# Optimization experiments

Measured on AMD Instinct MI355X. Metric: run time of the kernel, lower is better.

Reference implementation:

```python
import jax, jax.numpy as jnp
import numpy as np

N, F, H, E, R = 100000, 256, 64, 800000, 7
EPS = 1e-5

def _layernorm(x, g, b):
    mu = jnp.mean(x, axis=-1, keepdims=True)
    var = jnp.mean((x - mu) ** 2, axis=-1, keepdims=True)
    return (x - mu) * jax.lax.rsqrt(var + EPS) * g + b

def setup_inputs() -> dict:
    key = jax.random.key(0)
    ks = jax.random.split(key, 16)
    block_features = jax.random.normal(ks[0], (N, F), dtype=jnp.float32)
    src = jax.random.randint(ks[1], (E,), 0, N).astype(jnp.float32)
    dst = jax.random.randint(ks[2], (E,), 0, N).astype(jnp.float32)
    rel = jax.random.randint(ks[3], (E,), 0, R).astype(jnp.float32)
    w = jax.random.uniform(ks[4], (E,), dtype=jnp.float32)
    typed_edges = jnp.stack([src, dst, rel, w], axis=1)  # [E,4]
    def lin(k, fan_in, fan_out):
        s = 1.0 / np.sqrt(fan_in)
        k1, k2 = jax.random.split(k)
        return (jax.random.uniform(k1, (fan_in, fan_out), jnp.float32, -s, s),
                jax.random.uniform(k2, (fan_out,), jnp.float32, -s, s))
    W1, b1 = lin(ks[5], F, H)
    W2, b2 = lin(ks[6], H, H)
    rel_emb = jax.random.normal(ks[7], (R, H), dtype=jnp.float32)
    Wm1, bm1 = lin(ks[8], 3 * H + 1, H)
    Wm2, bm2 = lin(ks[9], H, H)
    Wg1, bg1 = lin(ks[10], 2 * H, H)
    Wg2, bg2 = lin(ks[11], H, H)
    return dict(block_features=block_features, typed_edges=typed_edges,
                W1=W1, b1=b1, g1=jnp.ones(H), be1=jnp.zeros(H), W2=W2, b2=b2,
                rel_emb=rel_emb, Wm1=Wm1, bm1=bm1, Wm2=Wm2, bm2=bm2,
                gn=jnp.ones(H), bn=jnp.zeros(H), Wg1=Wg1, bg1=bg1, Wg2=Wg2, bg2=bg2)

def reference(block_features, typed_edges, W1, b1, g1, be1, W2, b2, rel_emb,
              Wm1, bm1, Wm2, bm2, gn, bn, Wg1, bg1, Wg2, bg2):
    # node_proj: Linear -> LN -> ReLU -> Linear -> ReLU
    h = jax.nn.relu(_layernorm(block_features @ W1 + b1, g1, be1))
    h = jax.nn.relu(h @ W2 + b2)  # [N,H]
    src = typed_edges[:, 0].astype(jnp.int32)
    dst = typed_edges[:, 1].astype(jnp.int32)
    rel = typed_edges[:, 2].astype(jnp.int32)
    w = typed_edges[:, 3:4]  # [E,1]
    m_in = jnp.concatenate([h[src], h[dst], rel_emb[rel], w], axis=-1)  # [E,3H+1]
    msg = jax.nn.relu(m_in @ Wm1 + bm1) @ Wm2 + bm2  # [E,H]
    agg = jax.ops.segment_sum(msg, dst, num_segments=h.shape[0])  # [N,H]
    nodes = _layernorm(h + agg, gn, bn)
    g = jnp.concatenate([nodes.mean(axis=0), nodes.max(axis=0)], axis=-1)  # [2H]
    return jax.nn.relu(g @ Wg1 + bg1) @ Wg2 + bg2  # [H]
```

## Files before the change

kernel.cpp:

```cpp
#include <hip/hip_runtime.h>

typedef unsigned short u16;
typedef unsigned int   u32;
typedef __attribute__((ext_vector_type(8))) short bf16x8;
typedef __attribute__((ext_vector_type(4))) float f32x4;

#define EPS 1e-5f
#define MFMA(a,b,c) __builtin_amdgcn_mfma_f32_16x16x32_bf16(a,b,c,0,0,0)

constexpr int OB_b1=0, OB_g1=64, OB_be1=128, OB_b2=192, OB_bm1=256, OB_w192=320,
              OB_bm2=384, OB_gn=448, OB_bn=512, OB_bg1=576, OB_bg2=640,
              OB_Wg1=704, OB_Wg2=8896, WB_TOT=12992;
constexpr int FR_Wm1=0;
constexpr int FR_Wm2=12288;
constexpr int FR_rel=16384;
constexpr int FR_W1 =16960;
constexpr int FR_W2 =33344;
constexpr int FR_TOT=37440;

__device__ __forceinline__ float bf2f(u32 u) { return __uint_as_float(u << 16); }
__device__ __forceinline__ u16 f2bf(float f) {
  u32 b = __float_as_uint(f);
  return (u16)((b + 0x7fffu + ((b >> 16) & 1u)) >> 16);
}
__device__ __forceinline__ u32 fkey(float f) {
  u32 b = __float_as_uint(f);
  return (b & 0x80000000u) ? ~b : (b | 0x80000000u);
}

__launch_bounds__(256)
__global__ void k_prep(const float* __restrict__ W1, const float* __restrict__ b1,
                       const float* __restrict__ g1, const float* __restrict__ be1,
                       const float* __restrict__ W2, const float* __restrict__ b2,
                       const float* __restrict__ rel_emb,
                       const float* __restrict__ Wm1, const float* __restrict__ bm1,
                       const float* __restrict__ Wm2, const float* __restrict__ bm2,
                       const float* __restrict__ gn, const float* __restrict__ bn,
                       const float* __restrict__ Wg1, const float* __restrict__ bg1,
                       const float* __restrict__ Wg2, const float* __restrict__ bg2,
                       float* __restrict__ wbuf, u16* __restrict__ frags) {
  int tid = blockIdx.x * 256 + threadIdx.x;
  int nth = gridDim.x * 256;
  for (int i = tid; i < 64; i += nth) {
    wbuf[OB_b1 + i] = b1[i];   wbuf[OB_g1 + i] = g1[i];
    wbuf[OB_be1 + i] = be1[i]; wbuf[OB_b2 + i] = b2[i];
    wbuf[OB_bm1 + i] = bm1[i]; wbuf[OB_w192 + i] = Wm1[192 * 64 + i];
    wbuf[OB_bm2 + i] = bm2[i]; wbuf[OB_gn + i] = gn[i];
    wbuf[OB_bn + i] = bn[i];   wbuf[OB_bg1 + i] = bg1[i];
    wbuf[OB_bg2 + i] = bg2[i];
  }
  for (int i = tid; i < 8192; i += nth) wbuf[OB_Wg1 + i] = Wg1[i];
  for (int i = tid; i < 4096; i += nth) wbuf[OB_Wg2 + i] = Wg2[i];
  for (int idx = tid; idx < 16384; idx += nth) {
    int f = idx >> 9, L = (idx >> 3) & 63, j = idx & 7;
    int k = (f >> 2) * 32 + ((L >> 4) << 3) + j, n = ((f & 3) << 4) + (L & 15);
    frags[FR_W1 + idx] = f2bf(W1[k * 64 + n]);
  }
  for (int idx = tid; idx < 4096; idx += nth) {
    int f = idx >> 9, L = (idx >> 3) & 63, j = idx & 7;
    int k = (f >> 2) * 32 + ((L >> 4) << 3) + j, n = ((f & 3) << 4) + (L & 15);
    frags[FR_W2 + idx] = f2bf(W2[k * 64 + n]);
  }
  for (int idx = tid; idx < 12288; idx += nth) {
    int f = idx >> 9, L = (idx >> 3) & 63, j = idx & 7;
    int k = (f >> 2) * 32 + ((L >> 4) << 3) + j, n = ((f & 3) << 4) + (L & 15);
    frags[FR_Wm1 + idx] = f2bf(Wm1[k * 64 + n]);
  }
  for (int idx = tid; idx < 4096; idx += nth) {
    int f = idx >> 9, L = (idx >> 3) & 63, j = idx & 7;
    int k = (f >> 2) * 32 + ((L >> 4) << 3) + j, n = ((f & 3) << 4) + (L & 15);
    frags[FR_Wm2 + idx] = f2bf(Wm2[k * 64 + n]);
  }
  for (int idx = tid; idx < 576; idx += nth) {
    int r = idx / 80, c = idx % 80;
    frags[FR_rel + idx] = (r < 7 && c < 64) ? f2bf(rel_emb[r * 64 + c]) : (u16)0;
  }
}

__launch_bounds__(256, 3)
__global__ void k_h(const float* __restrict__ X, const float* __restrict__ wbuf,
                    const u16* __restrict__ frags, u16* __restrict__ hb, int N) {
  __shared__ __align__(16) u16 sW1[32 * 512];
  __shared__ __align__(16) u16 sW2[8 * 512];
  __shared__ __align__(16) u16 st[4][16 * 72];

  {
    const uint4* srcp = (const uint4*)(frags + FR_W1);
    uint4* d1 = (uint4*)sW1;
    for (int i = threadIdx.x; i < 2048; i += 256) d1[i] = srcp[i];
    const uint4* srcp2 = (const uint4*)(frags + FR_W2);
    uint4* d2 = (uint4*)sW2;
    for (int i = threadIdx.x; i < 512; i += 256) d2[i] = srcp2[i];
  }
  __syncthreads();

  int lane = threadIdx.x & 63, wave = threadIdx.x >> 6;
  int m = lane & 15, quad = lane >> 4, koff = quad * 8, col0 = m;

  float b1v[4], g1v[4], be1v[4], b2v[4];
  #pragma unroll
  for (int nt = 0; nt < 4; nt++) {
    int c = nt * 16 + col0;
    b1v[nt] = wbuf[OB_b1 + c]; g1v[nt] = wbuf[OB_g1 + c];
    be1v[nt] = wbuf[OB_be1 + c]; b2v[nt] = wbuf[OB_b2 + c];
  }

  int ntiles = (N + 15) / 16;
  int wid = blockIdx.x * 4 + wave, nw = gridDim.x * 4;
  for (int tile = wid; tile < ntiles; tile += nw) {
    int n0 = tile * 16;
    int nm = min(n0 + m, N - 1);
    const float* xr = X + (size_t)nm * 256 + koff;

    f32x4 acc[4] = {};
    #pragma unroll 1
    for (int ks = 0; ks < 8; ks++) {
      float4 u0 = *(const float4*)(xr + ks * 32);
      float4 u1 = *(const float4*)(xr + ks * 32 + 4);
      bf16x8 a;
      a[0] = (short)f2bf(u0.x); a[1] = (short)f2bf(u0.y);
      a[2] = (short)f2bf(u0.z); a[3] = (short)f2bf(u0.w);
      a[4] = (short)f2bf(u1.x); a[5] = (short)f2bf(u1.y);
      a[6] = (short)f2bf(u1.z); a[7] = (short)f2bf(u1.w);
      #pragma unroll
      for (int nt = 0; nt < 4; nt++) {
        bf16x8 b = *(const bf16x8*)(sW1 + (ks * 4 + nt) * 512 + lane * 8);
        acc[nt] = MFMA(a, b, acc[nt]);
      }
    }

    float v[4][4];
    #pragma unroll
    for (int nt = 0; nt < 4; nt++)
      #pragma unroll
      for (int r = 0; r < 4; r++) v[nt][r] = acc[nt][r] + b1v[nt];

    #pragma unroll
    for (int r = 0; r < 4; r++) {
      float s = v[0][r] + v[1][r] + v[2][r] + v[3][r];
      #pragma unroll
      for (int mk = 8; mk >= 1; mk >>= 1) s += __shfl_xor(s, mk, 64);
      float mu = s * (1.f / 64.f);
      float q = 0.f;
      #pragma unroll
      for (int nt = 0; nt < 4; nt++) { float d = v[nt][r] - mu; q += d * d; }
      #pragma unroll
      for (int mk = 8; mk >= 1; mk >>= 1) q += __shfl_xor(q, mk, 64);
      float rs = rsqrtf(q * (1.f / 64.f) + EPS);
      #pragma unroll
      for (int nt = 0; nt < 4; nt++) {
        float h1 = fmaxf(fmaf((v[nt][r] - mu) * rs, g1v[nt], be1v[nt]), 0.f);
        st[wave][(quad * 4 + r) * 72 + nt * 16 + col0] = f2bf(h1);
      }
    }
    __builtin_amdgcn_wave_barrier();

    f32x4 acc2[4] = {};
    #pragma unroll
    for (int ks = 0; ks < 2; ks++) {
      bf16x8 a2 = *(const bf16x8*)(st[wave] + m * 72 + ks * 32 + koff);
      #pragma unroll
      for (int nt = 0; nt < 4; nt++) {
        bf16x8 b = *(const bf16x8*)(sW2 + (ks * 4 + nt) * 512 + lane * 8);
        acc2[nt] = MFMA(a2, b, acc2[nt]);
      }
    }
    __builtin_amdgcn_wave_barrier();

    #pragma unroll
    for (int nt = 0; nt < 4; nt++)
      #pragma unroll
      for (int r = 0; r < 4; r++) {
        int row = n0 + quad * 4 + r;
        if (row < N)
          hb[(size_t)row * 64 + nt * 16 + col0] = f2bf(fmaxf(acc2[nt][r] + b2v[nt], 0.f));
      }
  }
}

__launch_bounds__(256, 3)
__global__ void k_edge(const float* __restrict__ te, const u16* __restrict__ hb,
                       const float* __restrict__ wbuf, const u16* __restrict__ frags,
                       float* __restrict__ agg, int E, int N) {
  __shared__ __align__(16) u16 sWm1[24 * 512];
  __shared__ __align__(16) u16 sWm2[8 * 512];
  __shared__ __align__(16) u16 srel[576];
  __shared__ __align__(16) u16 st[4][16 * 72];

  {
    const uint4* s1 = (const uint4*)(frags + FR_Wm1);
    uint4* d1 = (uint4*)sWm1;
    for (int i = threadIdx.x; i < 1536; i += 256) d1[i] = s1[i];
    const uint4* s2 = (const uint4*)(frags + FR_Wm2);
    uint4* d2 = (uint4*)sWm2;
    for (int i = threadIdx.x; i < 512; i += 256) d2[i] = s2[i];
    const uint4* s3 = (const uint4*)(frags + FR_rel);
    uint4* d3 = (uint4*)srel;
    for (int i = threadIdx.x; i < 72; i += 256) d3[i] = s3[i];
  }
  __syncthreads();

  int lane = threadIdx.x & 63, wave = threadIdx.x >> 6;
  int m = lane & 15, quad = lane >> 4, koff = quad * 8, col0 = m;

  float bm1v[4], w192v[4], bm2v[4];
  #pragma unroll
  for (int nt = 0; nt < 4; nt++) {
    int c = nt * 16 + col0;
    bm1v[nt] = wbuf[OB_bm1 + c];
    w192v[nt] = wbuf[OB_w192 + c];
    bm2v[nt] = wbuf[OB_bm2 + c];
  }

  int ntiles = (E + 15) / 16;
  int wid = blockIdx.x * 4 + wave, nw = gridDim.x * 4;
  for (int tile = wid; tile < ntiles; tile += nw) {
    int e0 = tile * 16;
    int src = 0, dst = 0, rel = 0; float w = 0.f;
    if (lane < 16) {
      int e = min(e0 + lane, E - 1);
      float4 v = *(const float4*)(te + (size_t)e * 4);
      src = min(max((int)v.x, 0), N - 1);
      dst = min(max((int)v.y, 0), N - 1);
      rel = min(max((int)v.z, 0), 6);
      w = v.w;
    }
    int src_m = __shfl(src, m, 64);
    int dst_m = __shfl(dst, m, 64);
    int rel_m = __shfl(rel, m, 64);

    const u16* hs = hb + (size_t)src_m * 64;
    const u16* hd = hb + (size_t)dst_m * 64;
    bf16x8 af[6];
    af[0] = *(const bf16x8*)(hs + koff);
    af[1] = *(const bf16x8*)(hs + 32 + koff);
    af[2] = *(const bf16x8*)(hd + koff);
    af[3] = *(const bf16x8*)(hd + 32 + koff);
    af[4] = *(const bf16x8*)(srel + rel_m * 80 + koff);
    af[5] = *(const bf16x8*)(srel + rel_m * 80 + 32 + koff);

    f32x4 acc[4] = {};
    #pragma unroll
    for (int ks = 0; ks < 6; ks++) {
      #pragma unroll
      for (int nt = 0; nt < 4; nt++) {
        bf16x8 b = *(const bf16x8*)(sWm1 + (ks * 4 + nt) * 512 + lane * 8);
        acc[nt] = MFMA(af[ks], b, acc[nt]);
      }
    }

    float wrow[4];
    #pragma unroll
    for (int r = 0; r < 4; r++) wrow[r] = __shfl(w, quad * 4 + r, 64);
    #pragma unroll
    for (int nt = 0; nt < 4; nt++)
      #pragma unroll
      for (int r = 0; r < 4; r++) {
        float v = fmaf(wrow[r], w192v[nt], acc[nt][r] + bm1v[nt]);
        st[wave][(quad * 4 + r) * 72 + nt * 16 + col0] = f2bf(fmaxf(v, 0.f));
      }
    __builtin_amdgcn_wave_barrier();

    f32x4 acc2[4] = {};
    #pragma unroll
    for (int ks = 0; ks < 2; ks++) {
      bf16x8 a2 = *(const bf16x8*)(st[wave] + m * 72 + ks * 32 + koff);
      #pragma unroll
      for (int nt = 0; nt < 4; nt++) {
        bf16x8 b = *(const bf16x8*)(sWm2 + (ks * 4 + nt) * 512 + lane * 8);
        acc2[nt] = MFMA(a2, b, acc2[nt]);
      }
    }
    __builtin_amdgcn_wave_barrier();

    int dstr[4]; bool valr[4];
    #pragma unroll
    for (int r = 0; r < 4; r++) {
      int row = quad * 4 + r;
      dstr[r] = __shfl(dst, row, 64);
      valr[r] = (e0 + row) < E;
    }
    #pragma unroll
    for (int nt = 0; nt < 4; nt++)
      #pragma unroll
      for (int r = 0; r < 4; r++)
        if (valr[r])
          atomicAdd(agg + (size_t)dstr[r] * 64 + nt * 16 + col0, acc2[nt][r] + bm2v[nt]);
  }
}

__launch_bounds__(256)
__global__ void k_nodes(const u16* __restrict__ hb, const float* __restrict__ agg,
                        const float* __restrict__ wbuf, float* __restrict__ gsum,
                        u32* __restrict__ gmax, int N) {
  int lane = threadIdx.x & 63, wave = threadIdx.x >> 6;
  int wid = blockIdx.x * 4 + wave;
  int nw = gridDim.x * 4;
  float gn = wbuf[OB_gn + lane], bn = wbuf[OB_bn + lane];
  float sj = 0.f, mj = -3.0e38f;
  for (int n = wid; n < N; n += nw) {
    float v = bf2f(hb[(size_t)n * 64 + lane]) + agg[(size_t)n * 64 + lane];
    float s = v;
    #pragma unroll
    for (int m = 32; m >= 1; m >>= 1) s += __shfl_xor(s, m, 64);
    float mu = s * (1.f / 64.f);
    float d = v - mu;
    float q = d * d;
    #pragma unroll
    for (int m = 32; m >= 1; m >>= 1) q += __shfl_xor(q, m, 64);
    float rs = rsqrtf(q * (1.f / 64.f) + EPS);
    float val = fmaf(d * rs, gn, bn);
    sj += val;
    mj = fmaxf(mj, val);
  }
  __shared__ float bs[256], bm[256];
  bs[threadIdx.x] = sj;
  bm[threadIdx.x] = mj;
  __syncthreads();
  if (threadIdx.x < 64) {
    int t = threadIdx.x;
    float ts = bs[t] + bs[64 + t] + bs[128 + t] + bs[192 + t];
    float tm = fmaxf(fmaxf(bm[t], bm[64 + t]), fmaxf(bm[128 + t], bm[192 + t]));
    atomicAdd(gsum + t, ts);
    atomicMax(gmax + t, fkey(tm));
  }
}

__launch_bounds__(128)
__global__ void k_final(const float* __restrict__ wbuf, const float* __restrict__ gsum,
                        const u32* __restrict__ gmax, float* __restrict__ out, int N) {
  __shared__ float g[128];
  __shared__ float y1[64];
  int t = threadIdx.x;
  if (t < 64) {
    g[t] = gsum[t] / (float)N;
  } else {
    u32 k = gmax[t - 64];
    u32 b = (k & 0x80000000u) ? (k & 0x7fffffffu) : ~k;
    g[t] = __uint_as_float(b);
  }
  __syncthreads();
  if (t < 64) {
    float a = wbuf[OB_bg1 + t];
    for (int i = 0; i < 128; i++) a = fmaf(g[i], wbuf[OB_Wg1 + i * 64 + t], a);
    y1[t] = fmaxf(a, 0.f);
  }
  __syncthreads();
  if (t < 64) {
    float a = wbuf[OB_bg2 + t];
    for (int k = 0; k < 64; k++) a = fmaf(y1[k], wbuf[OB_Wg2 + k * 64 + t], a);
    out[t] = a;
  }
}

extern "C" void kernel_launch(void* const* d_in, const int* in_sizes, int n_in,
                              void* d_out, int out_size, void* d_ws, size_t ws_size,
                              hipStream_t stream) {
  const int N = in_sizes[0] / 256;
  const int E = in_sizes[1] / 4;

  char* ws = (char*)d_ws;
  size_t aggB = (size_t)N * 64 * 4;
  size_t hbB  = (size_t)N * 64 * 2;
  float* agg   = (float*)ws;
  u16*   hb    = (u16*)(ws + aggB);
  float* gsum  = (float*)(ws + aggB + hbB);
  u32*   gmax  = (u32*)(ws + aggB + hbB + 256);
  float* wbuf  = (float*)(ws + aggB + hbB + 512);
  u16*   frags = (u16*)(ws + aggB + hbB + 512 + (size_t)WB_TOT * 4);

  const float* X  = (const float*)d_in[0];
  const float* te = (const float*)d_in[1];

  hipLaunchKernelGGL(k_prep, dim3(64), dim3(256), 0, stream,
                     (const float*)d_in[2], (const float*)d_in[3], (const float*)d_in[4],
                     (const float*)d_in[5], (const float*)d_in[6], (const float*)d_in[7],
                     (const float*)d_in[8], (const float*)d_in[9], (const float*)d_in[10],
                     (const float*)d_in[11], (const float*)d_in[12], (const float*)d_in[13],
                     (const float*)d_in[14], (const float*)d_in[15], (const float*)d_in[16],
                     (const float*)d_in[17], (const float*)d_in[18], wbuf, frags);
  hipMemsetAsync(agg, 0, aggB, stream);
  hipMemsetAsync(gsum, 0, 512, stream);
  hipLaunchKernelGGL(k_h, dim3(640), dim3(256), 0, stream, X, wbuf, frags, hb, N);
  hipLaunchKernelGGL(k_edge, dim3(768), dim3(256), 0, stream, te, hb, wbuf, frags, agg, E, N);
  hipLaunchKernelGGL(k_nodes, dim3(2048), dim3(256), 0, stream, hb, agg, wbuf, gsum, gmax, N);
  hipLaunchKernelGGL(k_final, dim3(1), dim3(128), 0, stream, wbuf, gsum, gmax, (float*)d_out, N);
}
```

Baseline: 442.6 us.

## Sort edges by destination and reduce runs before scattering aggregates

Edges are counted per destination, prefix-scanned and permuted into destination order. Each wave then accumulates contiguous same-destination messages in registers and issues one store or atomic per run, replacing one atomic per element. The prep kernel is dropped: weights are swizzled into shared memory inside each consumer kernel, the final MLP is folded into the last block of the node kernel, and the memsets are merged into one. The risk is the extra count, scan and permute passes, a single-block serial scan over 100k nodes, and messages rounded to bf16 before summation.

```diff
diff --git a/kernel.cpp b/kernel.cpp
--- a/kernel.cpp
+++ b/kernel.cpp
@@ -8,16 +8,6 @@
 #define EPS 1e-5f
 #define MFMA(a,b,c) __builtin_amdgcn_mfma_f32_16x16x32_bf16(a,b,c,0,0,0)
 
-constexpr int OB_b1=0, OB_g1=64, OB_be1=128, OB_b2=192, OB_bm1=256, OB_w192=320,
-              OB_bm2=384, OB_gn=448, OB_bn=512, OB_bg1=576, OB_bg2=640,
-              OB_Wg1=704, OB_Wg2=8896, WB_TOT=12992;
-constexpr int FR_Wm1=0;
-constexpr int FR_Wm2=12288;
-constexpr int FR_rel=16384;
-constexpr int FR_W1 =16960;
-constexpr int FR_W2 =33344;
-constexpr int FR_TOT=37440;
-
 __device__ __forceinline__ float bf2f(u32 u) { return __uint_as_float(u << 16); }
 __device__ __forceinline__ u16 f2bf(float f) {
   u32 b = __float_as_uint(f);
@@ -28,70 +18,28 @@
   return (b & 0x80000000u) ? ~b : (b | 0x80000000u);
 }
 
-__launch_bounds__(256)
-__global__ void k_prep(const float* __restrict__ W1, const float* __restrict__ b1,
-                       const float* __restrict__ g1, const float* __restrict__ be1,
-                       const float* __restrict__ W2, const float* __restrict__ b2,
-                       const float* __restrict__ rel_emb,
-                       const float* __restrict__ Wm1, const float* __restrict__ bm1,
-                       const float* __restrict__ Wm2, const float* __restrict__ bm2,
-                       const float* __restrict__ gn, const float* __restrict__ bn,
-                       const float* __restrict__ Wg1, const float* __restrict__ bg1,
-                       const float* __restrict__ Wg2, const float* __restrict__ bg2,
-                       float* __restrict__ wbuf, u16* __restrict__ frags) {
-  int tid = blockIdx.x * 256 + threadIdx.x;
-  int nth = gridDim.x * 256;
-  for (int i = tid; i < 64; i += nth) {
-    wbuf[OB_b1 + i] = b1[i];   wbuf[OB_g1 + i] = g1[i];
-    wbuf[OB_be1 + i] = be1[i]; wbuf[OB_b2 + i] = b2[i];
-    wbuf[OB_bm1 + i] = bm1[i]; wbuf[OB_w192 + i] = Wm1[192 * 64 + i];
-    wbuf[OB_bm2 + i] = bm2[i]; wbuf[OB_gn + i] = gn[i];
-    wbuf[OB_bn + i] = bn[i];   wbuf[OB_bg1 + i] = bg1[i];
-    wbuf[OB_bg2 + i] = bg2[i];
-  }
-  for (int i = tid; i < 8192; i += nth) wbuf[OB_Wg1 + i] = Wg1[i];
-  for (int i = tid; i < 4096; i += nth) wbuf[OB_Wg2 + i] = Wg2[i];
-  for (int idx = tid; idx < 16384; idx += nth) {
+__device__ __forceinline__ void swizzleW(const float* __restrict__ W, u16* __restrict__ s,
+                                         int nelem, int tid, int nthr) {
+  for (int idx = tid; idx < nelem; idx += nthr) {
     int f = idx >> 9, L = (idx >> 3) & 63, j = idx & 7;
     int k = (f >> 2) * 32 + ((L >> 4) << 3) + j, n = ((f & 3) << 4) + (L & 15);
-    frags[FR_W1 + idx] = f2bf(W1[k * 64 + n]);
-  }
-  for (int idx = tid; idx < 4096; idx += nth) {
-    int f = idx >> 9, L = (idx >> 3) & 63, j = idx & 7;
-    int k = (f >> 2) * 32 + ((L >> 4) << 3) + j, n = ((f & 3) << 4) + (L & 15);
-    frags[FR_W2 + idx] = f2bf(W2[k * 64 + n]);
-  }
-  for (int idx = tid; idx < 12288; idx += nth) {
-    int f = idx >> 9, L = (idx >> 3) & 63, j = idx & 7;
-    int k = (f >> 2) * 32 + ((L >> 4) << 3) + j, n = ((f & 3) << 4) + (L & 15);
-    frags[FR_Wm1 + idx] = f2bf(Wm1[k * 64 + n]);
-  }
-  for (int idx = tid; idx < 4096; idx += nth) {
-    int f = idx >> 9, L = (idx >> 3) & 63, j = idx & 7;
-    int k = (f >> 2) * 32 + ((L >> 4) << 3) + j, n = ((f & 3) << 4) + (L & 15);
-    frags[FR_Wm2 + idx] = f2bf(Wm2[k * 64 + n]);
-  }
-  for (int idx = tid; idx < 576; idx += nth) {
-    int r = idx / 80, c = idx % 80;
-    frags[FR_rel + idx] = (r < 7 && c < 64) ? f2bf(rel_emb[r * 64 + c]) : (u16)0;
+    s[idx] = f2bf(W[k * 64 + n]);
   }
 }
 
 __launch_bounds__(256, 3)
-__global__ void k_h(const float* __restrict__ X, const float* __restrict__ wbuf,
-                    const u16* __restrict__ frags, u16* __restrict__ hb, int N) {
+__global__ void k_h(const float* __restrict__ X,
+                    const float* __restrict__ W1, const float* __restrict__ b1,
+                    const float* __restrict__ g1, const float* __restrict__ be1,
+                    const float* __restrict__ W2, const float* __restrict__ b2,
+                    const float* __restrict__ te, u32* __restrict__ counts,
+                    u16* __restrict__ hb, int N, int E) {
   __shared__ __align__(16) u16 sW1[32 * 512];
   __shared__ __align__(16) u16 sW2[8 * 512];
   __shared__ __align__(16) u16 st[4][16 * 72];
 
-  {
-    const uint4* srcp = (const uint4*)(frags + FR_W1);
-    uint4* d1 = (uint4*)sW1;
-    for (int i = threadIdx.x; i < 2048; i += 256) d1[i] = srcp[i];
-    const uint4* srcp2 = (const uint4*)(frags + FR_W2);
-    uint4* d2 = (uint4*)sW2;
-    for (int i = threadIdx.x; i < 512; i += 256) d2[i] = srcp2[i];
-  }
+  swizzleW(W1, sW1, 16384, threadIdx.x, 256);
+  swizzleW(W2, sW2, 4096, threadIdx.x, 256);
   __syncthreads();
 
   int lane = threadIdx.x & 63, wave = threadIdx.x >> 6;
@@ -101,8 +49,7 @@
   #pragma unroll
   for (int nt = 0; nt < 4; nt++) {
     int c = nt * 16 + col0;
-    b1v[nt] = wbuf[OB_b1 + c]; g1v[nt] = wbuf[OB_g1 + c];
-    be1v[nt] = wbuf[OB_be1 + c]; b2v[nt] = wbuf[OB_b2 + c];
+    b1v[nt] = b1[c]; g1v[nt] = g1[c]; be1v[nt] = be1[c]; b2v[nt] = b2[c];
   }
 
   int ntiles = (N + 15) / 16;
@@ -113,7 +60,7 @@
     const float* xr = X + (size_t)nm * 256 + koff;
 
     f32x4 acc[4] = {};
-    #pragma unroll 1
+    #pragma unroll 4
     for (int ks = 0; ks < 8; ks++) {
       float4 u0 = *(const float4*)(xr + ks * 32);
       float4 u1 = *(const float4*)(xr + ks * 32 + 4);
@@ -176,27 +123,67 @@
           hb[(size_t)row * 64 + nt * 16 + col0] = f2bf(fmaxf(acc2[nt][r] + b2v[nt], 0.f));
       }
   }
+
+  int tid = blockIdx.x * 256 + threadIdx.x;
+  int nth = gridDim.x * 256;
+  for (int e = tid; e < E; e += nth) {
+    float dv = te[(size_t)e * 4 + 1];
+    int d = min(max((int)dv, 0), N - 1);
+    atomicAdd(&counts[d], 1u);
+  }
+}
+
+__launch_bounds__(1024)
+__global__ void k_scan(const u32* __restrict__ counts, u32* __restrict__ cursor, int M) {
+  __shared__ u32 sh[1024];
+  int tid = threadIdx.x;
+  int per = (M + 1023) >> 10;
+  int lo = tid * per, hi = min(lo + per, M);
+  u32 s = 0;
+  for (int i = lo; i < hi; i++) s += counts[i];
+  sh[tid] = s;
+  __syncthreads();
+  for (int off = 1; off < 1024; off <<= 1) {
+    u32 v = (tid >= off) ? sh[tid - off] : 0u;
+    __syncthreads();
+    sh[tid] += v;
+    __syncthreads();
+  }
+  u32 base = (tid > 0) ? sh[tid - 1] : 0u;
+  for (int i = lo; i < hi; i++) { u32 c = counts[i]; cursor[i] = base; base += c; }
+}
+
+__launch_bounds__(256)
+__global__ void k_perm(const float* __restrict__ te, u32* __restrict__ cursor,
+                       uint4* __restrict__ tes, int E, int N) {
+  int tid = blockIdx.x * 256 + threadIdx.x;
+  int nth = gridDim.x * 256;
+  for (int e = tid; e < E; e += nth) {
+    float4 v = *(const float4*)(te + (size_t)e * 4);
+    int s = min(max((int)v.x, 0), N - 1);
+    int d = min(max((int)v.y, 0), N - 1);
+    int r = min(max((int)v.z, 0), 6);
+    u32 pos = atomicAdd(&cursor[d], 1u);
+    tes[pos] = make_uint4((u32)s, (u32)d, (u32)r, __float_as_uint(v.w));
+  }
 }
 
 __launch_bounds__(256, 3)
-__global__ void k_edge(const float* __restrict__ te, const u16* __restrict__ hb,
-                       const float* __restrict__ wbuf, const u16* __restrict__ frags,
-                       float* __restrict__ agg, int E, int N) {
+__global__ void k_edge(const uint4* __restrict__ tes, const u16* __restrict__ hb,
+                       const float* __restrict__ Wm1, const float* __restrict__ bm1,
+                       const float* __restrict__ Wm2, const float* __restrict__ bm2,
+                       const float* __restrict__ rel_emb,
+                       float* __restrict__ agg, int E, int N, int nranges) {
   __shared__ __align__(16) u16 sWm1[24 * 512];
   __shared__ __align__(16) u16 sWm2[8 * 512];
   __shared__ __align__(16) u16 srel[576];
   __shared__ __align__(16) u16 st[4][16 * 72];
 
-  {
-    const uint4* s1 = (const uint4*)(frags + FR_Wm1);
-    uint4* d1 = (uint4*)sWm1;
-    for (int i = threadIdx.x; i < 1536; i += 256) d1[i] = s1[i];
-    const uint4* s2 = (const uint4*)(frags + FR_Wm2);
-    uint4* d2 = (uint4*)sWm2;
-    for (int i = threadIdx.x; i < 512; i += 256) d2[i] = s2[i];
-    const uint4* s3 = (const uint4*)(frags + FR_rel);
-    uint4* d3 = (uint4*)srel;
-    for (int i = threadIdx.x; i < 72; i += 256) d3[i] = s3[i];
+  swizzleW(Wm1, sWm1, 12288, threadIdx.x, 256);
+  swizzleW(Wm2, sWm2, 4096, threadIdx.x, 256);
+  for (int idx = threadIdx.x; idx < 576; idx += 256) {
+    int r = idx / 80, c = idx % 80;
+    srel[idx] = (r < 7 && c < 64) ? f2bf(rel_emb[r * 64 + c]) : (u16)0;
   }
   __syncthreads();
 
@@ -207,96 +194,120 @@
   #pragma unroll
   for (int nt = 0; nt < 4; nt++) {
     int c = nt * 16 + col0;
-    bm1v[nt] = wbuf[OB_bm1 + c];
-    w192v[nt] = wbuf[OB_w192 + c];
-    bm2v[nt] = wbuf[OB_bm2 + c];
-  }
-
-  int ntiles = (E + 15) / 16;
+    bm1v[nt] = bm1[c];
+    w192v[nt] = Wm1[192 * 64 + c];
+    bm2v[nt] = bm2[c];
+  }
+
   int wid = blockIdx.x * 4 + wave, nw = gridDim.x * 4;
-  for (int tile = wid; tile < ntiles; tile += nw) {
-    int e0 = tile * 16;
-    int src = 0, dst = 0, rel = 0; float w = 0.f;
-    if (lane < 16) {
-      int e = min(e0 + lane, E - 1);
-      float4 v = *(const float4*)(te + (size_t)e * 4);
-      src = min(max((int)v.x, 0), N - 1);
-      dst = min(max((int)v.y, 0), N - 1);
-      rel = min(max((int)v.z, 0), 6);
-      w = v.w;
-    }
-    int src_m = __shfl(src, m, 64);
-    int dst_m = __shfl(dst, m, 64);
-    int rel_m = __shfl(rel, m, 64);
-
-    const u16* hs = hb + (size_t)src_m * 64;
-    const u16* hd = hb + (size_t)dst_m * 64;
-    bf16x8 af[6];
-    af[0] = *(const bf16x8*)(hs + koff);
-    af[1] = *(const bf16x8*)(hs + 32 + koff);
-    af[2] = *(const bf16x8*)(hd + koff);
-    af[3] = *(const bf16x8*)(hd + 32 + koff);
-    af[4] = *(const bf16x8*)(srel + rel_m * 80 + koff);
-    af[5] = *(const bf16x8*)(srel + rel_m * 80 + 32 + koff);
-
-    f32x4 acc[4] = {};
-    #pragma unroll
-    for (int ks = 0; ks < 6; ks++) {
-      #pragma unroll
-      for (int nt = 0; nt < 4; nt++) {
-        bf16x8 b = *(const bf16x8*)(sWm1 + (ks * 4 + nt) * 512 + lane * 8);
-        acc[nt] = MFMA(af[ks], b, acc[nt]);
-      }
-    }
-
-    float wrow[4];
-    #pragma unroll
-    for (int r = 0; r < 4; r++) wrow[r] = __shfl(w, quad * 4 + r, 64);
-    #pragma unroll
-    for (int nt = 0; nt < 4; nt++)
-      #pragma unroll
-      for (int r = 0; r < 4; r++) {
-        float v = fmaf(wrow[r], w192v[nt], acc[nt][r] + bm1v[nt]);
-        st[wave][(quad * 4 + r) * 72 + nt * 16 + col0] = f2bf(fmaxf(v, 0.f));
-      }
-    __builtin_amdgcn_wave_barrier();
-
-    f32x4 acc2[4] = {};
-    #pragma unroll
-    for (int ks = 0; ks < 2; ks++) {
-      bf16x8 a2 = *(const bf16x8*)(st[wave] + m * 72 + ks * 32 + koff);
-      #pragma unroll
-      for (int nt = 0; nt < 4; nt++) {
-        bf16x8 b = *(const bf16x8*)(sWm2 + (ks * 4 + nt) * 512 + lane * 8);
-        acc2[nt] = MFMA(a2, b, acc2[nt]);
-      }
-    }
-    __builtin_amdgcn_wave_barrier();
-
-    int dstr[4]; bool valr[4];
-    #pragma unroll
-    for (int r = 0; r < 4; r++) {
-      int row = quad * 4 + r;
-      dstr[r] = __shfl(dst, row, 64);
-      valr[r] = (e0 + row) < E;
-    }
-    #pragma unroll
-    for (int nt = 0; nt < 4; nt++)
-      #pragma unroll
-      for (int r = 0; r < 4; r++)
-        if (valr[r])
-          atomicAdd(agg + (size_t)dstr[r] * 64 + nt * 16 + col0, acc2[nt][r] + bm2v[nt]);
+  for (int range = wid; range < nranges; range += nw) {
+    int r0 = range * 128;
+    int run_dst = -2;
+    float run = 0.f;
+    bool bs = false;
+
+    #pragma unroll 1
+    for (int t8 = 0; t8 < 8; t8++) {
+      int p0 = r0 + t8 * 16;
+      if (p0 >= E) break;
+
+      int src = 0, dstc = 0, rel = 0, dtag = -1; float w = 0.f;
+      if (lane < 16) {
+        int p = p0 + lane;
+        if (p < E) {
+          uint4 v = tes[p];
+          src = (int)v.x; dstc = (int)v.y; rel = (int)v.z;
+          w = __uint_as_float(v.w);
+          dtag = dstc;
+        }
+      }
+      int src_m = __shfl(src, m, 64);
+      int dst_m = __shfl(dstc, m, 64);
+      int rel_m = __shfl(rel, m, 64);
+
+      const u16* hs = hb + (size_t)src_m * 64;
+      const u16* hd = hb + (size_t)dst_m * 64;
+      bf16x8 af[6];
+      af[0] = *(const bf16x8*)(hs + koff);
+      af[1] = *(const bf16x8*)(hs + 32 + koff);
+      af[2] = *(const bf16x8*)(hd + koff);
+      af[3] = *(const bf16x8*)(hd + 32 + koff);
+      af[4] = *(const bf16x8*)(srel + rel_m * 80 + koff);
+      af[5] = *(const bf16x8*)(srel + rel_m * 80 + 32 + koff);
+
+      f32x4 acc[4] = {};
+      #pragma unroll
+      for (int ks = 0; ks < 6; ks++) {
+        #pragma unroll
+        for (int nt = 0; nt < 4; nt++) {
+          bf16x8 b = *(const bf16x8*)(sWm1 + (ks * 4 + nt) * 512 + lane * 8);
+          acc[nt] = MFMA(af[ks], b, acc[nt]);
+        }
+      }
+
+      float wrow[4];
+      #pragma unroll
+      for (int r = 0; r < 4; r++) wrow[r] = __shfl(w, quad * 4 + r, 64);
+      #pragma unroll
+      for (int nt = 0; nt < 4; nt++)
+        #pragma unroll
+        for (int r = 0; r < 4; r++) {
+          float v = fmaf(wrow[r], w192v[nt], acc[nt][r] + bm1v[nt]);
+          st[wave][(quad * 4 + r) * 72 + nt * 16 + col0] = f2bf(fmaxf(v, 0.f));
+        }
+      __builtin_amdgcn_wave_barrier();
+
+      f32x4 acc2[4] = {};
+      #pragma unroll
+      for (int ks = 0; ks < 2; ks++) {
+        bf16x8 a2 = *(const bf16x8*)(st[wave] + m * 72 + ks * 32 + koff);
+        #pragma unroll
+        for (int nt = 0; nt < 4; nt++) {
+          bf16x8 b = *(const bf16x8*)(sWm2 + (ks * 4 + nt) * 512 + lane * 8);
+          acc2[nt] = MFMA(a2, b, acc2[nt]);
+        }
+      }
+      __builtin_amdgcn_wave_barrier();
+
+      #pragma unroll
+      for (int nt = 0; nt < 4; nt++)
+        #pragma unroll
+        for (int r = 0; r < 4; r++)
+          st[wave][(quad * 4 + r) * 72 + nt * 16 + col0] =
+              f2bf(acc2[nt][r] + bm2v[nt]);
+      __builtin_amdgcn_wave_barrier();
+
+      #pragma unroll 1
+      for (int r = 0; r < 16; r++) {
+        int d = __shfl(dtag, r, 64);
+        float val = bf2f(st[wave][r * 72 + lane]);
+        if (d != run_dst) {
+          if (run_dst >= 0) {
+            float* ap = agg + (size_t)run_dst * 64 + lane;
+            if (bs) atomicAdd(ap, run); else *ap = run;
+          }
+          run_dst = d; run = val; bs = (t8 == 0 && r == 0);
+        } else {
+          run += val;
+        }
+      }
+      __builtin_amdgcn_wave_barrier();
+    }
+    if (run_dst >= 0) atomicAdd(agg + (size_t)run_dst * 64 + lane, run);
   }
 }
 
 __launch_bounds__(256)
 __global__ void k_nodes(const u16* __restrict__ hb, const float* __restrict__ agg,
-                        const float* __restrict__ wbuf, float* __restrict__ gsum,
-                        u32* __restrict__ gmax, int N) {
+                        const float* __restrict__ gn, const float* __restrict__ bn,
+                        const float* __restrict__ Wg1, const float* __restrict__ bg1,
+                        const float* __restrict__ Wg2, const float* __restrict__ bg2,
+                        float* __restrict__ gsum, u32* __restrict__ gmax,
+                        u32* __restrict__ done, float* __restrict__ out, int N) {
   int lane = threadIdx.x & 63, wave = threadIdx.x >> 6;
   int wid = blockIdx.x * 4 + wave;
   int nw = gridDim.x * 4;
-  float gn = wbuf[OB_gn + lane], bn = wbuf[OB_bn + lane];
+  float gnv = gn[lane], bnv = bn[lane];
   float sj = 0.f, mj = -3.0e38f;
   for (int n = wid; n < N; n += nw) {
     float v = bf2f(hb[(size_t)n * 64 + lane]) + agg[(size_t)n * 64 + lane];
@@ -309,7 +320,7 @@
     #pragma unroll
     for (int m = 32; m >= 1; m >>= 1) q += __shfl_xor(q, m, 64);
     float rs = rsqrtf(q * (1.f / 64.f) + EPS);
-    float val = fmaf(d * rs, gn, bn);
+    float val = fmaf(d * rs, gnv, bnv);
     sj += val;
     mj = fmaxf(mj, val);
   }
@@ -324,32 +335,35 @@
     atomicAdd(gsum + t, ts);
     atomicMax(gmax + t, fkey(tm));
   }
-}
-
-__launch_bounds__(128)
-__global__ void k_final(const float* __restrict__ wbuf, const float* __restrict__ gsum,
-                        const u32* __restrict__ gmax, float* __restrict__ out, int N) {
-  __shared__ float g[128];
-  __shared__ float y1[64];
-  int t = threadIdx.x;
-  if (t < 64) {
-    g[t] = gsum[t] / (float)N;
-  } else {
-    u32 k = gmax[t - 64];
-    u32 b = (k & 0x80000000u) ? (k & 0x7fffffffu) : ~k;
-    g[t] = __uint_as_float(b);
-  }
+
+  __threadfence();
+  __shared__ u32 lastv;
+  if (threadIdx.x == 0) lastv = atomicAdd(done, 1u);
   __syncthreads();
-  if (t < 64) {
-    float a = wbuf[OB_bg1 + t];
-    for (int i = 0; i < 128; i++) a = fmaf(g[i], wbuf[OB_Wg1 + i * 64 + t], a);
-    y1[t] = fmaxf(a, 0.f);
-  }
-  __syncthreads();
-  if (t < 64) {
-    float a = wbuf[OB_bg2 + t];
-    for (int k = 0; k < 64; k++) a = fmaf(y1[k], wbuf[OB_Wg2 + k * 64 + t], a);
-    out[t] = a;
+  if (lastv == gridDim.x - 1) {
+    __shared__ float g[128];
+    __shared__ float y1[64];
+    int t = threadIdx.x;
+    if (t < 64) {
+      float sv = __hip_atomic_load(&gsum[t], __ATOMIC_RELAXED, __HIP_MEMORY_SCOPE_AGENT);
+      g[t] = sv / (float)N;
+    } else if (t < 128) {
+      u32 k = __hip_atomic_load(&gmax[t - 64], __ATOMIC_RELAXED, __HIP_MEMORY_SCOPE_AGENT);
+      u32 b = (k & 0x80000000u) ? (k & 0x7fffffffu) : ~k;
+      g[t] = __uint_as_float(b);
+    }
+    __syncthreads();
+    if (t < 64) {
+      float a = bg1[t];
+      for (int i = 0; i < 128; i++) a = fmaf(g[i], Wg1[i * 64 + t], a);
+      y1[t] = fmaxf(a, 0.f);
+    }
+    __syncthreads();
+    if (t < 64) {
+      float a = bg2[t];
+      for (int k = 0; k < 64; k++) a = fmaf(y1[k], Wg2[k * 64 + t], a);
+      out[t] = a;
+    }
   }
 }
 
@@ -358,31 +372,36 @@
                               hipStream_t stream) {
   const int N = in_sizes[0] / 256;
   const int E = in_sizes[1] / 4;
-
-  char* ws = (char*)d_ws;
-  size_t aggB = (size_t)N * 64 * 4;
-  size_t hbB  = (size_t)N * 64 * 2;
-  float* agg   = (float*)ws;
-  u16*   hb    = (u16*)(ws + aggB);
-  float* gsum  = (float*)(ws + aggB + hbB);
-  u32*   gmax  = (u32*)(ws + aggB + hbB + 256);
-  float* wbuf  = (float*)(ws + aggB + hbB + 512);
-  u16*   frags = (u16*)(ws + aggB + hbB + 512 + (size_t)WB_TOT * 4);
+  const int Mp = (N + 63) & ~63;
+
+  float* agg    = (float*)d_ws;
+  float* gsum   = agg + (size_t)N * 64;
+  u32*   gmax   = (u32*)(gsum + 64);
+  u32*   done   = gmax + 64;
+  u32*   counts = done + 64;
+  u32*   cursor = counts + Mp;
+  uint4* tes    = (uint4*)(cursor + Mp);
+  u16*   hb     = (u16*)(tes + E);
+  size_t zeroB  = ((size_t)N * 64 + 192 + Mp) * 4;
 
   const float* X  = (const float*)d_in[0];
   const float* te = (const float*)d_in[1];
 
-  hipLaunchKernelGGL(k_prep, dim3(64), dim3(256), 0, stream,
+  hipMemsetAsync(agg, 0, zeroB, stream);
+  hipLaunchKernelGGL(k_h, dim3(800), dim3(256), 0, stream, X,
                      (const float*)d_in[2], (const float*)d_in[3], (const float*)d_in[4],
                      (const float*)d_in[5], (const float*)d_in[6], (const float*)d_in[7],
-                     (const float*)d_in[8], (const float*)d_in[9], (const float*)d_in[10],
-                     (const float*)d_in[11], (const float*)d_in[12], (const float*)d_in[13],
-                     (const float*)d_in[14], (const float*)d_in[15], (const float*)d_in[16],
-                     (const float*)d_in[17], (const float*)d_in[18], wbuf, frags);
-  hipMemsetAsync(agg, 0, aggB, stream);
-  hipMemsetAsync(gsum, 0, 512, stream);
-  hipLaunchKernelGGL(k_h, dim3(640), dim3(256), 0, stream, X, wbuf, frags, hb, N);
-  hipLaunchKernelGGL(k_edge, dim3(768), dim3(256), 0, stream, te, hb, wbuf, frags, agg, E, N);
-  hipLaunchKernelGGL(k_nodes, dim3(2048), dim3(256), 0, stream, hb, agg, wbuf, gsum, gmax, N);
-  hipLaunchKernelGGL(k_final, dim3(1), dim3(128), 0, stream, wbuf, gsum, gmax, (float*)d_out, N);
-}
+                     te, counts, hb, N, E);
+  hipLaunchKernelGGL(k_scan, dim3(1), dim3(1024), 0, stream, counts, cursor, N);
+  hipLaunchKernelGGL(k_perm, dim3(800), dim3(256), 0, stream, te, cursor, tes, E, N);
+  int nranges = (E + 127) / 128;
+  hipLaunchKernelGGL(k_edge, dim3(768), dim3(256), 0, stream, tes, hb,
+                     (const float*)d_in[9], (const float*)d_in[10],
+                     (const float*)d_in[11], (const float*)d_in[12],
+                     (const float*)d_in[8], agg, E, N, nranges);
+  hipLaunchKernelGGL(k_nodes, dim3(2048), dim3(256), 0, stream, hb, agg,
+                     (const float*)d_in[13], (const float*)d_in[14],
+                     (const float*)d_in[15], (const float*)d_in[16],
+                     (const float*)d_in[17], (const float*)d_in[18],
+                     gsum, gmax, done, (float*)d_out, N);
+}
```

New measurement: 717.1 us. +62.0%, slower.
